# Kernel optimization log

Hardware: AMD Instinct MI355X
Metric: run time of the kernel (lower is better)

## Reference

```python
import jax, jax.numpy as jnp
import numpy as np

N = 8192   # number of points (p) == number of reference points (r); must match for final bmm
D = 1024   # feature width of the Linear projections


def setup_inputs() -> dict:
    key = jax.random.key(0)
    ks = jax.random.split(key, 8)
    s = 1.0 / np.sqrt(D)
    return {
        "p": jax.random.normal(ks[0], (N, D), dtype=jnp.float32),
        "r": jax.random.normal(ks[1], (N, D), dtype=jnp.float32),
        "Wh": jax.random.uniform(ks[2], (D, D), jnp.float32, -s, s),
        "bh": jax.random.uniform(ks[3], (D,), jnp.float32, -s, s),
        "Wl": jax.random.uniform(ks[4], (D, D), jnp.float32, -s, s),
        "bl": jax.random.uniform(ks[5], (D,), jnp.float32, -s, s),
        "Wg": jax.random.uniform(ks[6], (D, D), jnp.float32, -s, s),
        "bg": jax.random.uniform(ks[7], (D,), jnp.float32, -s, s),
    }


def reference(p, r, Wh, bh, Wl, bl, Wg, bg):
    # Linear projections (torch Linear: x @ W.T + b)
    q = p @ Wh.T + bh          # [N, D]  M_h(p)
    k = r @ Wl.T + bl          # [N, D]  M_l(r)
    v = p @ Wg.T + bg          # [N, D]  M_g(p)
    scores = q @ k.T           # [N, N]  == bmm(q[None], k[None].transpose(1,2))[0]
    # torch softmax dim=1 on [1, N, N] normalizes over the QUERY axis -> axis=0 here
    attn = jax.nn.softmax(scores, axis=0)
    return p + attn @ v        # residual add
```

## Files before the change

### kernel.cpp

```cpp
#include <hip/hip_runtime.h>
#include <hip/hip_fp16.h>

typedef _Float16 f16;
typedef __attribute__((ext_vector_type(8))) _Float16 f16x8;
typedef __attribute__((ext_vector_type(4))) float f32x4;

#define NPTS 8192
#define DIM  1024
#define HL2E 0.721347520444482f
#define S2SHIFT 50.0f
#define TBUF (128 * 32)

__device__ __forceinline__ void glds16(const void* g, void* l) {
  __builtin_amdgcn_global_load_lds(
      (const __attribute__((address_space(1))) void*)g,
      (__attribute__((address_space(3))) void*)l, 16, 0, 0);
}


__global__ void cvt_f32_f16(const float* __restrict__ src, f16* __restrict__ dst, int n) {
  int i = (blockIdx.x * 256 + threadIdx.x) * 8;
  if (i >= n) return;
  const float4* s = (const float4*)(src + i);
  float4 a = s[0], b = s[1];
  f16x8 o;
  o[0] = (f16)a.x; o[1] = (f16)a.y; o[2] = (f16)a.z; o[3] = (f16)a.w;
  o[4] = (f16)b.x; o[5] = (f16)b.y; o[6] = (f16)b.z; o[7] = (f16)b.w;
  *(f16x8*)(dst + i) = o;
}

__global__ void zero_f32(float* __restrict__ p, int n) {
  int i = blockIdx.x * 256 + threadIdx.x;
  if (i < n) p[i] = 0.f;
}

__global__ void mk_scales(const float* __restrict__ colsum,
                          f16* __restrict__ ics2, f16* __restrict__ ics4) {
  int j = blockIdx.x * 256 + threadIdx.x;
  float r2 = rsqrtf(colsum[j]);
  ics2[j] = (f16)r2;
  ics4[j] = (f16)sqrtf(r2);
}

__global__ void vscale(f16* __restrict__ vt, const f16* __restrict__ ics2) {
  long i = ((long)blockIdx.x * 256 + threadIdx.x) * 8;
  f16x8 v = *(f16x8*)(vt + i);
  f16x8 s = *(const f16x8*)(ics2 + (i & (NPTS - 1)));
  *(f16x8*)(vt + i) = v * s;
}

__global__ void reduce_out(const float* __restrict__ p,
                           const float* __restrict__ pa,
                           const float* __restrict__ pb,
                           float* __restrict__ out) {
  long i = ((long)blockIdx.x * 256 + threadIdx.x) * 4;
  float4 a = *(const float4*)(p + i);
  float4 b = *(const float4*)(pa + i);
  float4 c = *(const float4*)(pb + i);
  a.x += b.x + c.x; a.y += b.y + c.y; a.z += b.z + c.z; a.w += b.w + c.w;
  *(float4*)(out + i) = a;
}

__global__ __launch_bounds__(256, 2)
void proj_fused(const f16* __restrict__ p_h, const f16* __restrict__ r_h,
                const f16* __restrict__ Wh, const f16* __restrict__ Wl,
                const f16* __restrict__ Wg,
                const float* __restrict__ bh, const float* __restrict__ bl,
                const float* __restrict__ bg,
                f16* __restrict__ q_h, f16* __restrict__ k_h,
                f16* __restrict__ vt_h) {
  __shared__ f16 sA[2 * TBUF];
  __shared__ f16 sB[2 * TBUF];
  const int sub = blockIdx.x >> 9;
  const int bl_ = blockIdx.x & 511;
  const long bi = (long)(bl_ & 63) * 128;
  const long bj = (long)(bl_ >> 6) * 128;
  const f16* A = (sub == 1) ? r_h : p_h;
  const f16* B = (sub == 0) ? Wh : (sub == 1) ? Wl : Wg;
  const float* bias = (sub == 0) ? bh : (sub == 1) ? bl : bg;

  const int t = threadIdx.x;
  const int w = t >> 6, l = t & 63;
  const int wm = (w >> 1) * 64, wn = (w & 1) * 64;
  const int lr = l & 15;
  const int fbase = lr * 32 + (((l >> 4) ^ ((lr >> 1) & 3)) * 8);
  const int grow = w * 16 + (l >> 2);
  const int gcol = ((l & 3) ^ ((l >> 3) & 3)) * 8;
  const f16* gA = A + (bi + grow) * (long)DIM + gcol;
  const f16* gB = B + (bj + grow) * (long)DIM + gcol;
  const int lw0 = (w * 16) * 32, lw1 = (64 + w * 16) * 32;

  glds16(gA, sA + lw0);
  glds16(gA + 64l * DIM, sA + lw1);
  glds16(gB, sB + lw0);
  glds16(gB + 64l * DIM, sB + lw1);
  gA += 32; gB += 32;

  f32x4 acc[4][4] = {};
  const int nk = DIM / 32;
  for (int k = 0; k < nk; k++) {
    const int cur = (k & 1) * TBUF, nxt = TBUF - cur;
    __syncthreads();
    if (k + 1 < nk) {
      glds16(gA, sA + nxt + lw0);
      glds16(gA + 64l * DIM, sA + nxt + lw1);
      glds16(gB, sB + nxt + lw0);
      glds16(gB + 64l * DIM, sB + nxt + lw1);
      gA += 32; gB += 32;
    }
    f16x8 af[4], bf[4];
#pragma unroll
    for (int mt = 0; mt < 4; mt++)
      af[mt] = *(const f16x8*)(sA + cur + (wm + mt * 16) * 32 + fbase);
#pragma unroll
    for (int nt = 0; nt < 4; nt++)
      bf[nt] = *(const f16x8*)(sB + cur + (wn + nt * 16) * 32 + fbase);
#pragma unroll
    for (int mt = 0; mt < 4; mt++)
#pragma unroll
      for (int nt = 0; nt < 4; nt++)
        acc[mt][nt] = __builtin_amdgcn_mfma_f32_16x16x32_f16(af[mt], bf[nt], acc[mt][nt], 0, 0, 0);
  }

  const int rbase = (l >> 4) * 4;
  f16* C = (sub == 0) ? q_h : (sub == 1) ? k_h : vt_h;
#pragma unroll
  for (int nt = 0; nt < 4; nt++) {
    const long col = bj + wn + nt * 16 + lr;
    const float bb = bias[col];
#pragma unroll
    for (int mt = 0; mt < 4; mt++) {
      const long row0 = bi + wm + mt * 16 + rbase;
      if (sub < 2) {
#pragma unroll
        for (int g = 0; g < 4; g++)
          C[(row0 + g) * DIM + col] = (f16)(acc[mt][nt][g] + bb);
      } else {
        union { unsigned long long u; f16 h[4]; } pk;
#pragma unroll
        for (int g = 0; g < 4; g++) pk.h[g] = (f16)(acc[mt][nt][g] + bb);
        *(unsigned long long*)(C + col * (long)NPTS + row0) = pk.u;
      }
    }
  }
}

__global__ __launch_bounds__(256, 2)
void gemm_qk(const f16* __restrict__ A, const f16* __restrict__ B,
             f16* __restrict__ S, float* __restrict__ colsum) {
  __shared__ f16 sA[2 * TBUF];
  __shared__ f16 sB[2 * TBUF];
  const int b = blockIdx.x;
  const int sx = b & 7;
  const int j = b >> 3;
  const int st = j >> 6;
  const int wi = j & 63;
  const long bi = (long)(st * 8 + (wi >> 3)) * 128;
  const long bj = (long)(sx * 8 + (wi & 7)) * 128;
  const int t = threadIdx.x;
  const int w = t >> 6, l = t & 63;
  const int wm = (w >> 1) * 64, wn = (w & 1) * 64;
  const int lr = l & 15;
  const int fbase = lr * 32 + (((l >> 4) ^ ((lr >> 1) & 3)) * 8);
  const int grow = w * 16 + (l >> 2);
  const int gcol = ((l & 3) ^ ((l >> 3) & 3)) * 8;
  const f16* gA = A + (bi + grow) * (long)DIM + gcol;
  const f16* gB = B + (bj + grow) * (long)DIM + gcol;
  const int lw0 = (w * 16) * 32, lw1 = (64 + w * 16) * 32;

  glds16(gA, sA + lw0);
  glds16(gA + 64l * DIM, sA + lw1);
  glds16(gB, sB + lw0);
  glds16(gB + 64l * DIM, sB + lw1);
  gA += 32; gB += 32;

  f32x4 acc[4][4] = {};
  const int nk = DIM / 32;
  for (int k = 0; k < nk; k++) {
    const int cur = (k & 1) * TBUF, nxt = TBUF - cur;
    __syncthreads();
    if (k + 1 < nk) {
      glds16(gA, sA + nxt + lw0);
      glds16(gA + 64l * DIM, sA + nxt + lw1);
      glds16(gB, sB + nxt + lw0);
      glds16(gB + 64l * DIM, sB + nxt + lw1);
      gA += 32; gB += 32;
    }
    f16x8 af[4], bf[4];
#pragma unroll
    for (int mt = 0; mt < 4; mt++)
      af[mt] = *(const f16x8*)(sA + cur + (wm + mt * 16) * 32 + fbase);
#pragma unroll
    for (int nt = 0; nt < 4; nt++)
      bf[nt] = *(const f16x8*)(sB + cur + (wn + nt * 16) * 32 + fbase);
#pragma unroll
    for (int mt = 0; mt < 4; mt++)
#pragma unroll
      for (int nt = 0; nt < 4; nt++)
        acc[mt][nt] = __builtin_amdgcn_mfma_f32_16x16x32_f16(af[mt], bf[nt], acc[mt][nt], 0, 0, 0);
  }

  const int rbase = (l >> 4) * 4;
#pragma unroll
  for (int nt = 0; nt < 4; nt++) {
    const long col = bj + wn + nt * 16 + lr;
    float csum = 0.f;
#pragma unroll
    for (int mt = 0; mt < 4; mt++) {
      const long row0 = bi + wm + mt * 16 + rbase;
#pragma unroll
      for (int g = 0; g < 4; g++) {
        float e = exp2f((acc[mt][nt][g] - S2SHIFT) * HL2E);
        e = fminf(e, 240.f);
        f16 eh = (f16)e;
        S[(row0 + g) * NPTS + col] = eh;
        float ef = (float)eh;
        csum += ef * ef;
      }
    }
    csum += __shfl_xor(csum, 16);
    csum += __shfl_xor(csum, 32);
    if (l < 16) atomicAdd(colsum + col, csum);
  }
}

__global__ __launch_bounds__(256, 2)
void gemm_pv(const f16* __restrict__ Sm, const f16* __restrict__ vt,
             const f16* __restrict__ ics4,
             float* __restrict__ part0, float* __restrict__ part1) {
  __shared__ f16 sA[2 * TBUF];
  __shared__ f16 sB[2 * TBUF];
  const int split = blockIdx.x >> 9;
  const int bl_ = blockIdx.x & 511;
  const long bi = (long)(bl_ & 63) * 128;
  const long bj = (long)(bl_ >> 6) * 128;
  const long koff = (long)split * (NPTS / 2);

  const int t = threadIdx.x;
  const int w = t >> 6, l = t & 63;
  const int wm = (w >> 1) * 64, wn = (w & 1) * 64;
  const int lr = l & 15;
  const int fbase = lr * 32 + (((l >> 4) ^ ((lr >> 1) & 3)) * 8);
  const int grow = w * 16 + (l >> 2);
  const int gcol = ((l & 3) ^ ((l >> 3) & 3)) * 8;
  const f16* gB = vt + (bj + grow) * (long)NPTS + koff + gcol;
  const int lw0 = (w * 16) * 32, lw1 = (64 + w * 16) * 32;

  const int sr = t >> 2, sc = (t & 3) * 8;
  const int ssw = ((t & 3) ^ ((t >> 3) & 3)) * 8;
  const f16* gAs = Sm + (bi + sr) * (long)NPTS + koff + sc;
  const f16* gIc = ics4 + koff + sc;
  f16x8 ra0, ra1, icv;

  const int nk = (NPTS / 2) / 32;

  ra0 = *(const f16x8*)gAs;
  ra1 = *(const f16x8*)(gAs + 64l * NPTS);
  icv = *(const f16x8*)gIc;
  {
    f16x8 t0 = ra0 * icv; t0 = t0 * t0;
    f16x8 t1 = ra1 * icv; t1 = t1 * t1;
    *(f16x8*)(sA + sr * 32 + ssw) = t0;
    *(f16x8*)(sA + (sr + 64) * 32 + ssw) = t1;
  }
  gAs += 32; gIc += 32;
  ra0 = *(const f16x8*)gAs;
  ra1 = *(const f16x8*)(gAs + 64l * NPTS);
  icv = *(const f16x8*)gIc;
  glds16(gB, sB + lw0);
  glds16(gB + 64l * NPTS, sB + lw1);
  gB += 32;

  f32x4 acc[4][4] = {};
  for (int k = 0; k < nk; k++) {
    const int cur = (k & 1) * TBUF, nxt = TBUF - cur;
    __syncthreads();
    if (k + 1 < nk) {
      f16x8 t0 = ra0 * icv; t0 = t0 * t0;
      f16x8 t1 = ra1 * icv; t1 = t1 * t1;
      *(f16x8*)(sA + nxt + sr * 32 + ssw) = t0;
      *(f16x8*)(sA + nxt + (sr + 64) * 32 + ssw) = t1;
      if (k + 2 < nk) {
        gAs += 32; gIc += 32;
        ra0 = *(const f16x8*)gAs;
        ra1 = *(const f16x8*)(gAs + 64l * NPTS);
        icv = *(const f16x8*)gIc;
      }
      glds16(gB, sB + nxt + lw0);
      glds16(gB + 64l * NPTS, sB + nxt + lw1);
      gB += 32;
    }
    f16x8 af[4], bf[4];
#pragma unroll
    for (int mt = 0; mt < 4; mt++)
      af[mt] = *(const f16x8*)(sA + cur + (wm + mt * 16) * 32 + fbase);
#pragma unroll
    for (int nt = 0; nt < 4; nt++)
      bf[nt] = *(const f16x8*)(sB + cur + (wn + nt * 16) * 32 + fbase);
#pragma unroll
    for (int mt = 0; mt < 4; mt++)
#pragma unroll
      for (int nt = 0; nt < 4; nt++)
        acc[mt][nt] = __builtin_amdgcn_mfma_f32_16x16x32_f16(af[mt], bf[nt], acc[mt][nt], 0, 0, 0);
  }

  float* part = split ? part1 : part0;
  const int rbase = (l >> 4) * 4;
#pragma unroll
  for (int nt = 0; nt < 4; nt++) {
    const long col = bj + wn + nt * 16 + lr;
#pragma unroll
    for (int mt = 0; mt < 4; mt++) {
      const long row0 = bi + wm + mt * 16 + rbase;
#pragma unroll
      for (int g = 0; g < 4; g++)
        part[(row0 + g) * DIM + col] = acc[mt][nt][g];
    }
  }
}

extern "C" void kernel_launch(void* const* d_in, const int* in_sizes, int n_in,
                              void* d_out, int out_size, void* d_ws, size_t ws_size,
                              hipStream_t stream) {
  const float* p  = (const float*)d_in[0];
  const float* r  = (const float*)d_in[1];
  const float* Wh = (const float*)d_in[2];
  const float* bh = (const float*)d_in[3];
  const float* Wl = (const float*)d_in[4];
  const float* bl = (const float*)d_in[5];
  const float* Wg = (const float*)d_in[6];
  const float* bg = (const float*)d_in[7];
  float* out = (float*)d_out;

  char* ws = (char*)d_ws;
  f16* q_h  = (f16*)(ws + (0ull  << 20));
  f16* k_h  = (f16*)(ws + (16ull << 20));
  f16* vt_h = (f16*)(ws + (32ull << 20));
  f16* p_h  = (f16*)(ws + (48ull << 20));
  f16* r_h  = (f16*)(ws + (64ull << 20));
  f16* wh_h = (f16*)(ws + (80ull << 20));
  f16* wl_h = (f16*)(ws + (82ull << 20));
  f16* wg_h = (f16*)(ws + (84ull << 20));
  f16* S    = (f16*)(ws + (96ull << 20));
  float* colsum = (float*)(ws + (224ull << 20));
  f16* ics2 = (f16*)(ws + (225ull << 20));
  f16* ics4 = (f16*)(ws + (226ull << 20));
  float* part0 = (float*)(ws + (0ull  << 20));
  float* part1 = (float*)(ws + (48ull << 20));

  const int nP = NPTS * DIM, nW = DIM * DIM;
  cvt_f32_f16<<<nP / 2048, 256, 0, stream>>>(p,  p_h,  nP);
  cvt_f32_f16<<<nP / 2048, 256, 0, stream>>>(r,  r_h,  nP);
  cvt_f32_f16<<<nW / 2048, 256, 0, stream>>>(Wh, wh_h, nW);
  cvt_f32_f16<<<nW / 2048, 256, 0, stream>>>(Wl, wl_h, nW);
  cvt_f32_f16<<<nW / 2048, 256, 0, stream>>>(Wg, wg_h, nW);
  zero_f32<<<NPTS / 256, 256, 0, stream>>>(colsum, NPTS);

  dim3 blk(256);
  proj_fused<<<1536, blk, 0, stream>>>(p_h, r_h, wh_h, wl_h, wg_h,
                                       bh, bl, bg, q_h, k_h, vt_h);
  gemm_qk<<<4096, blk, 0, stream>>>(q_h, k_h, S, colsum);
  mk_scales<<<NPTS / 256, 256, 0, stream>>>(colsum, ics2, ics4);
  vscale<<<(NPTS / 8) * (DIM / 256), 256, 0, stream>>>(vt_h, ics2);
  gemm_pv<<<1024, blk, 0, stream>>>(S, vt_h, ics4, part0, part1);
  reduce_out<<<nP / 1024, 256, 0, stream>>>(p, part0, part1, out);
}
```

Before: 554.8 us.

## Retile QK GEMM to 256x256 blocks with 4-stage LDS pipeline

The QK score GEMM now uses 512-thread blocks computing 256x256 tiles instead of 256-thread 128x128 tiles, which cuts global reloads of q and k per output. The K loop becomes a 4-buffer, 3-deep prefetch pipeline that splits each step into two MFMA halves interleaved with async global-to-LDS loads, using explicit waitcnt, barriers and setprio. This uses 128KB of LDS and doubles the accumulator registers, which may limit occupancy or cause spilling.

```diff
diff --git a/kernel.cpp b/kernel.cpp
--- a/kernel.cpp
+++ b/kernel.cpp
@@ -145,71 +145,95 @@
   }
 }
 
-__global__ __launch_bounds__(256, 2)
+__global__ __launch_bounds__(512, 2)
 void gemm_qk(const f16* __restrict__ A, const f16* __restrict__ B,
              f16* __restrict__ S, float* __restrict__ colsum) {
-  __shared__ f16 sA[2 * TBUF];
-  __shared__ f16 sB[2 * TBUF];
+  __shared__ f16 smem[4 * 16384];
   const int b = blockIdx.x;
   const int sx = b & 7;
   const int j = b >> 3;
-  const int st = j >> 6;
-  const int wi = j & 63;
-  const long bi = (long)(st * 8 + (wi >> 3)) * 128;
-  const long bj = (long)(sx * 8 + (wi & 7)) * 128;
+  const long bi = (long)(j >> 2) * 256;
+  const long bj = (long)(sx * 4 + (j & 3)) * 256;
+
   const int t = threadIdx.x;
   const int w = t >> 6, l = t & 63;
-  const int wm = (w >> 1) * 64, wn = (w & 1) * 64;
+  const int wm = (w >> 2) * 128, wn = (w & 3) * 64;
   const int lr = l & 15;
   const int fbase = lr * 32 + (((l >> 4) ^ ((lr >> 1) & 3)) * 8);
-  const int grow = w * 16 + (l >> 2);
-  const int gcol = ((l & 3) ^ ((l >> 3) & 3)) * 8;
-  const f16* gA = A + (bi + grow) * (long)DIM + gcol;
-  const f16* gB = B + (bj + grow) * (long)DIM + gcol;
-  const int lw0 = (w * 16) * 32, lw1 = (64 + w * 16) * 32;
-
-  glds16(gA, sA + lw0);
-  glds16(gA + 64l * DIM, sA + lw1);
-  glds16(gB, sB + lw0);
-  glds16(gB + 64l * DIM, sB + lw1);
-  gA += 32; gB += 32;
-
-  f32x4 acc[4][4] = {};
-  const int nk = DIM / 32;
-  for (int k = 0; k < nk; k++) {
-    const int cur = (k & 1) * TBUF, nxt = TBUF - cur;
-    __syncthreads();
-    if (k + 1 < nk) {
-      glds16(gA, sA + nxt + lw0);
-      glds16(gA + 64l * DIM, sA + nxt + lw1);
-      glds16(gB, sB + nxt + lw0);
-      glds16(gB + 64l * DIM, sB + nxt + lw1);
-      gA += 32; gB += 32;
-    }
-    f16x8 af[4], bf[4];
-#pragma unroll
-    for (int mt = 0; mt < 4; mt++)
-      af[mt] = *(const f16x8*)(sA + cur + (wm + mt * 16) * 32 + fbase);
-#pragma unroll
-    for (int nt = 0; nt < 4; nt++)
-      bf[nt] = *(const f16x8*)(sB + cur + (wn + nt * 16) * 32 + fbase);
-#pragma unroll
-    for (int mt = 0; mt < 4; mt++)
-#pragma unroll
-      for (int nt = 0; nt < 4; nt++)
+  const int sro = t >> 2;
+  const int scol = ((t & 3) ^ ((t >> 3) & 3)) * 8;
+  const f16* gAs = A + (bi + sro) * (long)DIM + scol;
+  const f16* gBs = B + (bj + sro) * (long)DIM + scol;
+  const int ldst = w * 512;
+
+#pragma unroll
+  for (int tl = 0; tl < 3; ++tl) {
+    f16* d = smem + tl * 16384;
+    glds16(gAs + tl * 32,              d + ldst);
+    glds16(gAs + tl * 32 + 128l * DIM, d + 4096 + ldst);
+    glds16(gBs + tl * 32,              d + 8192 + ldst);
+    glds16(gBs + tl * 32 + 128l * DIM, d + 12288 + ldst);
+  }
+  asm volatile("s_waitcnt vmcnt(8)" ::: "memory");
+  __builtin_amdgcn_s_barrier();
+
+  f32x4 acc[8][4] = {};
+  f16x8 bf[4];
+  for (int kt = 0; kt < 32; ++kt) {
+    const f16* sa = smem + (kt & 3) * 16384;
+    f16* d = smem + ((kt + 3) & 3) * 16384;
+    const int ks = (kt + 3 < 32) ? (kt + 3) : 31;
+    const f16* as_ = gAs + ks * 32;
+    const f16* bs_ = gBs + ks * 32;
+    f16x8 af[4];
+
+#pragma unroll
+    for (int mt = 0; mt < 4; ++mt)
+      af[mt] = *(const f16x8*)(sa + (wm + mt * 16) * 32 + fbase);
+#pragma unroll
+    for (int nt = 0; nt < 4; ++nt)
+      bf[nt] = *(const f16x8*)(sa + 8192 + (wn + nt * 16) * 32 + fbase);
+    glds16(as_,              d + ldst);
+    glds16(as_ + 128l * DIM, d + 4096 + ldst);
+    __builtin_amdgcn_s_barrier();
+    asm volatile("s_waitcnt lgkmcnt(0)" ::: "memory");
+    __builtin_amdgcn_s_setprio(1);
+#pragma unroll
+    for (int mt = 0; mt < 4; ++mt)
+#pragma unroll
+      for (int nt = 0; nt < 4; ++nt)
         acc[mt][nt] = __builtin_amdgcn_mfma_f32_16x16x32_f16(af[mt], bf[nt], acc[mt][nt], 0, 0, 0);
+    __builtin_amdgcn_s_setprio(0);
+    __builtin_amdgcn_s_barrier();
+
+#pragma unroll
+    for (int mt = 0; mt < 4; ++mt)
+      af[mt] = *(const f16x8*)(sa + (wm + 64 + mt * 16) * 32 + fbase);
+    glds16(bs_,              d + 8192 + ldst);
+    glds16(bs_ + 128l * DIM, d + 12288 + ldst);
+    __builtin_amdgcn_s_barrier();
+    asm volatile("s_waitcnt lgkmcnt(0)" ::: "memory");
+    __builtin_amdgcn_s_setprio(1);
+#pragma unroll
+    for (int mt = 0; mt < 4; ++mt)
+#pragma unroll
+      for (int nt = 0; nt < 4; ++nt)
+        acc[4 + mt][nt] = __builtin_amdgcn_mfma_f32_16x16x32_f16(af[mt], bf[nt], acc[4 + mt][nt], 0, 0, 0);
+    __builtin_amdgcn_s_setprio(0);
+    asm volatile("s_waitcnt vmcnt(8)" ::: "memory");
+    __builtin_amdgcn_s_barrier();
   }
 
   const int rbase = (l >> 4) * 4;
 #pragma unroll
-  for (int nt = 0; nt < 4; nt++) {
+  for (int nt = 0; nt < 4; ++nt) {
     const long col = bj + wn + nt * 16 + lr;
     float csum = 0.f;
 #pragma unroll
-    for (int mt = 0; mt < 4; mt++) {
+    for (int mt = 0; mt < 8; ++mt) {
       const long row0 = bi + wm + mt * 16 + rbase;
 #pragma unroll
-      for (int g = 0; g < 4; g++) {
+      for (int g = 0; g < 4; ++g) {
         float e = exp2f((acc[mt][nt][g] - S2SHIFT) * HL2E);
         e = fminf(e, 240.f);
         f16 eh = (f16)e;
@@ -359,7 +383,7 @@
   dim3 blk(256);
   proj_fused<<<1536, blk, 0, stream>>>(p_h, r_h, wh_h, wl_h, wg_h,
                                        bh, bl, bg, q_h, k_h, vt_h);
-  gemm_qk<<<4096, blk, 0, stream>>>(q_h, k_h, S, colsum);
+  gemm_qk<<<1024, dim3(512), 0, stream>>>(q_h, k_h, S, colsum);
   mk_scales<<<NPTS / 256, 256, 0, stream>>>(colsum, ics2, ics4);
   vscale<<<(NPTS / 8) * (DIM / 256), 256, 0, stream>>>(vt_h, ics2);
   gemm_pv<<<1024, blk, 0, stream>>>(S, vt_h, ics4, part0, part1);
```

After: 570.1 us. 2.8% more time.
